# Kernel optimization log

Measured on AMD Instinct MI355X. Metric: run time of the kernel, lower is better.

The kernel has to match this reference:

```python
import jax, jax.numpy as jnp
import numpy as np
import math

D_MODEL = 1024
N_HEAD = 16
D_K = 64
D_V = 64
EPS = 1e-6


def setup_inputs() -> dict:
    key = jax.random.key(0)
    ks = jax.random.split(key, 10)
    B, S = 4, 2048
    inp = {
        'x_queries': jax.random.normal(ks[0], (B, S, D_MODEL), jnp.float32),
        'x_keys': jax.random.normal(ks[1], (B, S, D_MODEL), jnp.float32),
        'x_values': jax.random.normal(ks[2], (B, S, D_MODEL), jnp.float32),
        'mask': jax.random.randint(ks[3], (B, S, S), 0, 2, jnp.int32),
        # Linear(d_model, n_head*d_k, bias=False) weights stored as [in, out]
        'w_q': jax.random.normal(ks[4], (D_MODEL, N_HEAD * D_K), jnp.float32) * np.sqrt(2.0 / (D_MODEL + D_K)),
        'w_k': jax.random.normal(ks[5], (D_MODEL, N_HEAD * D_K), jnp.float32) * np.sqrt(2.0 / (D_MODEL + D_K)),
        'w_v': jax.random.normal(ks[6], (D_MODEL, N_HEAD * D_V), jnp.float32) * np.sqrt(2.0 / (D_MODEL + D_V)),
        'w_0': jax.random.normal(ks[7], (N_HEAD * D_V, D_MODEL), jnp.float32) * np.sqrt(2.0 / (N_HEAD * D_V + D_MODEL)),
        'gamma': jnp.ones((D_MODEL,), jnp.float32),
        'beta': jnp.zeros((D_MODEL,), jnp.float32),
    }
    return inp


def _layer_norm(x, gamma, beta, eps=EPS):
    # Matches the torch module: std with Bessel correction, eps added to std.
    mean = jnp.mean(x, axis=-1, keepdims=True)
    std = jnp.std(x, axis=-1, keepdims=True, ddof=1)
    return gamma * (x - mean) / (std + eps) + beta


def reference(x_queries, x_keys, x_values, mask, w_q, w_k, w_v, w_0, gamma, beta):
    B, Lq, _ = x_queries.shape
    residual = x_queries
    # Projections -> [B, L, H, D]
    Q = (x_queries @ w_q).reshape(B, Lq, N_HEAD, D_K)
    K = (x_keys @ w_k).reshape(B, x_keys.shape[1], N_HEAD, D_K)
    V = (x_values @ w_v).reshape(B, x_values.shape[1], N_HEAD, D_V)
    # Scaled dot-product attention (scores materialized as in the original bmm path)
    scores = jnp.einsum('bqhd,bkhd->bhqk', Q, K) / math.sqrt(D_K)
    # NOTE: original masked_fill uses eps (not -inf) where mask == 0
    scores = jnp.where(mask[:, None, :, :] == 0, EPS, scores)
    attn = jax.nn.softmax(scores, axis=-1)
    out = jnp.einsum('bhqk,bkhd->bqhd', attn, V).reshape(B, Lq, N_HEAD * D_V)
    out = out @ w_0
    return _layer_norm(out + residual, gamma, beta)
```

## Files before the change

### kernel.cpp

```cpp
#include <hip/hip_runtime.h>
#include <hip/hip_bf16.h>
#include <math.h>

#define DM 1024
#define NH 16
#define DK 64
#define BB 4
#define SS 2048
#define EPSV 1e-6f
#define NE ((size_t)BB * SS * DM)
#define MM ((size_t)DM * DM)
#define QSCALE 0.18033688011112042f

typedef __attribute__((ext_vector_type(8))) short short8;
typedef __attribute__((ext_vector_type(4))) float f32x4;

__device__ inline unsigned short f2bf(float x) {
  unsigned int u = __builtin_bit_cast(unsigned int, x);
  u += 0x7FFF + ((u >> 16) & 1);
  return (unsigned short)(u >> 16);
}
__device__ inline ushort4 f2bf4(float4 v) {
  ushort4 r;
  r.x = f2bf(v.x); r.y = f2bf(v.y); r.z = f2bf(v.z); r.w = f2bf(v.w);
  return r;
}

__device__ inline float fexp2(float x) {
#if __has_builtin(__builtin_amdgcn_exp2f)
  return __builtin_amdgcn_exp2f(x);
#else
  return exp2f(x);
#endif
}

__device__ inline unsigned cvtpk_bf16(float a, float b) {
  unsigned r;
  asm("v_cvt_pk_bf16_f32 %0, %1, %2" : "=v"(r) : "v"(a), "v"(b));
  return r;
}

__device__ inline void gl_lds16(const unsigned short* g, unsigned short* l) {
  __builtin_amdgcn_global_load_lds((const __attribute__((address_space(1))) void*)g,
                                   (__attribute__((address_space(3))) void*)l, 16, 0, 0);
}

__global__ __launch_bounds__(256) void cvt_x_k(const float* __restrict__ xq,
                                               const float* __restrict__ xk,
                                               const float* __restrict__ xv,
                                               unsigned short* __restrict__ oq,
                                               unsigned short* __restrict__ ok,
                                               unsigned short* __restrict__ ov) {
  const size_t NF4 = NE / 4;
  size_t g = (size_t)blockIdx.x * 256 + threadIdx.x;
  int t = (int)(g / NF4);
  size_t i = g - (size_t)t * NF4;
  const float* s = (t == 0) ? xq : (t == 1) ? xk : xv;
  unsigned short* d = (t == 0) ? oq : (t == 1) ? ok : ov;
  float4 v = ((const float4*)s)[i];
  ((ushort4*)d)[i] = f2bf4(v);
}

__global__ __launch_bounds__(256) void cvt_wT_k(const float* __restrict__ w0,
                                                const float* __restrict__ w1,
                                                const float* __restrict__ w2,
                                                const float* __restrict__ w3,
                                                unsigned short* __restrict__ o0,
                                                unsigned short* __restrict__ o1,
                                                unsigned short* __restrict__ o2,
                                                unsigned short* __restrict__ o3) {
  __shared__ float t[32][33];
  int z = blockIdx.z;
  const float* w = (z == 0) ? w0 : (z == 1) ? w1 : (z == 2) ? w2 : w3;
  unsigned short* o = (z == 0) ? o0 : (z == 1) ? o1 : (z == 2) ? o2 : o3;
  float sc = (z == 0) ? QSCALE : 1.0f;
  int n0 = blockIdx.x * 32, k0 = blockIdx.y * 32;
  int tx = threadIdx.x & 31, ty = threadIdx.x >> 5;
#pragma unroll
  for (int s = 0; s < 4; ++s) t[ty + s * 8][tx] = w[(size_t)(k0 + ty + s * 8) * DM + n0 + tx];
  __syncthreads();
#pragma unroll
  for (int s = 0; s < 4; ++s)
    o[(size_t)(n0 + ty + s * 8) * DM + k0 + tx] = f2bf(t[tx][ty + s * 8] * sc);
}

__global__ __launch_bounds__(256) void maskbits_k(const int* __restrict__ mask,
                                                  unsigned long long* __restrict__ bm) {
  const int total = BB * SS * (SS / 64);
  int lane = threadIdx.x & 63;
  int wid = (blockIdx.x * 256 + threadIdx.x) >> 6;
  int nw = (gridDim.x * 256) >> 6;
  for (int w = wid; w < total; w += nw) {
    int v = mask[(size_t)w * 64 + lane];
    unsigned long long bal = __ballot(v != 0);
    if (lane == 0) bm[w] = bal;
  }
}

__global__ __launch_bounds__(256) void vpack_k(const unsigned short* __restrict__ Vb,
                                               unsigned short* __restrict__ VP) {
  __shared__ unsigned short t[64][72];
  int b = blockIdx.z, h = blockIdx.y, kt = blockIdx.x;
  int tid = threadIdx.x;
#pragma unroll
  for (int p = 0; p < 2; ++p) {
    int idx = p * 256 + tid;
    int r = idx >> 3, cch = (idx & 7) * 8;
    short8 v = *(const short8*)&Vb[((size_t)b * SS + kt * 64 + r) * DM + h * DK + cch];
    *(short8*)&t[r][cch] = v;
  }
  __syncthreads();
  int o = tid >> 4, w0 = o & 3;
  int dcol = (o >> 2) * 16 + ((tid & 15) >> 1) * 2 + (tid & 1);
  unsigned short* dst =
      VP + (((size_t)b * NH + h) * (SS / 64) + kt) * 4096 + (size_t)tid * 8;
#pragma unroll
  for (int p = 0; p < 2; ++p) {
    union { short8 v; unsigned short u[8]; } pk;
#pragma unroll
    for (int j = 0; j < 8; ++j) {
      int srow = p * 32 + 16 * (j >> 2) + 4 * w0 + (j & 3);
      pk.u[j] = t[srow][dcol];
    }
    *(short8*)&dst[p * 2048] = pk.v;
  }
}

template <bool BF16OUT>
__global__ __launch_bounds__(256) void gemm_lds_k(const unsigned short* __restrict__ Abase,
                                                  const unsigned short* __restrict__ WTbase,
                                                  void* __restrict__ Cv, int M, int N, int K,
                                                  size_t zA, size_t zW, size_t zC) {
  __shared__ __align__(16) unsigned short As[128 * 32];
  __shared__ __align__(16) unsigned short Bs[128 * 32];
  const unsigned short* A = Abase + (size_t)blockIdx.z * zA;
  const unsigned short* WT = WTbase + (size_t)blockIdx.z * zW;
  int bm = blockIdx.y * 128, bn = blockIdx.x * 128;
  int tid = threadIdx.x, lane = tid & 63, w = tid >> 6;
  int quad = lane >> 4, c = lane & 15, wx = w & 1, wy = w >> 1;

  f32x4 acc[4][4];
#pragma unroll
  for (int mt = 0; mt < 4; ++mt)
#pragma unroll
    for (int nt = 0; nt < 4; ++nt)
#pragma unroll
      for (int r = 0; r < 4; ++r) acc[mt][nt][r] = 0.f;

  int srow = lane >> 2, scol = (lane & 3) * 8;
  const unsigned short* Ag = A + (size_t)(bm + w * 32 + srow) * K + scol;
  const unsigned short* Bg = WT + (size_t)(bn + w * 32 + srow) * K + scol;
  unsigned short* Al = &As[w * 32 * 32];
  unsigned short* Bl = &Bs[w * 32 * 32];

  for (int k0 = 0; k0 < K; k0 += 32) {
    gl_lds16(Ag + k0, Al);
    gl_lds16(Ag + (size_t)16 * K + k0, Al + 16 * 32);
    gl_lds16(Bg + k0, Bl);
    gl_lds16(Bg + (size_t)16 * K + k0, Bl + 16 * 32);
    __syncthreads();
    short8 af[4], bf[4];
#pragma unroll
    for (int mt = 0; mt < 4; ++mt) af[mt] = *(const short8*)&As[(wy * 64 + mt * 16 + c) * 32 + quad * 8];
#pragma unroll
    for (int nt = 0; nt < 4; ++nt) bf[nt] = *(const short8*)&Bs[(wx * 64 + nt * 16 + c) * 32 + quad * 8];
#pragma unroll
    for (int mt = 0; mt < 4; ++mt)
#pragma unroll
      for (int nt = 0; nt < 4; ++nt)
        acc[mt][nt] = __builtin_amdgcn_mfma_f32_16x16x32_bf16(af[mt], bf[nt], acc[mt][nt], 0, 0, 0);
    __syncthreads();
  }
#pragma unroll
  for (int mt = 0; mt < 4; ++mt)
#pragma unroll
    for (int nt = 0; nt < 4; ++nt)
#pragma unroll
      for (int r = 0; r < 4; ++r) {
        size_t idx = (size_t)blockIdx.z * zC +
                     (size_t)(bm + wy * 64 + mt * 16 + quad * 4 + r) * N + bn + wx * 64 + nt * 16 + c;
        if (BF16OUT)
          ((unsigned short*)Cv)[idx] = f2bf(acc[mt][nt][r]);
        else
          ((float*)Cv)[idx] = acc[mt][nt][r];
      }
}

__global__ __launch_bounds__(256) void attn_mfma_k(const unsigned short* __restrict__ Q,
                                                   const unsigned short* __restrict__ Kg,
                                                   const unsigned short* __restrict__ VP,
                                                   const unsigned long long* __restrict__ bm,
                                                   unsigned short* __restrict__ O) {
  __shared__ __align__(16) unsigned short Ks[2][64 * 64];
  __shared__ __align__(16) unsigned short Vs[2][64 * 64];
  int b = blockIdx.z, h = blockIdx.y, q0 = blockIdx.x * 64;
  int tid = threadIdx.x, lane = tid & 63, w = tid >> 6;
  int quad = lane >> 4, c = lane & 15;

  short8 qf[2];
  {
    const unsigned short* qp = Q + ((size_t)b * SS + q0 + w * 16 + c) * DM + h * DK + quad * 8;
    qf[0] = *(const short8*)qp;
    qf[1] = *(const short8*)(qp + 32);
  }
  const unsigned long long* bp = bm + ((size_t)b * SS + q0 + w * 16 + c) * (SS / 64);
  const int shq = quad * 4;

  short8 ones8;
#pragma unroll
  for (int j = 0; j < 8; ++j) ones8[j] = (short)0x3F80;

  f32x4 accO[4], lacc;
#pragma unroll
  for (int r = 0; r < 4; ++r) lacc[r] = 0.f;
#pragma unroll
  for (int dt = 0; dt < 4; ++dt)
#pragma unroll
    for (int r = 0; r < 4; ++r) accO[dt][r] = 0.f;

  int kr = tid >> 3;
  int scc = (tid & 7) ^ (kr & 7);
  const unsigned short* pK0 = Kg + ((size_t)b * SS + kr) * DM + h * DK + scc * 8;
  const unsigned short* pK1 = pK0 + (size_t)32 * DM;
  const unsigned short* pV0 =
      VP + ((size_t)b * NH + h) * (SS / 64) * 4096 + (size_t)tid * 8;
  const unsigned short* pV1 = pV0 + 2048;

  const int kfo0 = c * 64 + ((quad ^ (c & 7)) * 8);
  const int kfo1 = c * 64 + (((4 + quad) ^ (c & 7)) * 8);
  const int vfbase = quad * 128 + c * 8;

  const int NT = SS / 64;

  gl_lds16(pK0, &Ks[0][w * 512]);
  gl_lds16(pK1, &Ks[0][2048 + w * 512]);
  gl_lds16(pV0, &Vs[0][w * 512]);
  gl_lds16(pV1, &Vs[0][2048 + w * 512]);
  pK0 += (size_t)64 * DM; pK1 += (size_t)64 * DM;
  pV0 += 4096; pV1 += 4096;
  unsigned long long mw = bp[0];

  auto tile = [&](int buf, int kt) {
    __syncthreads();
    if (kt + 1 < NT) {
      gl_lds16(pK0, &Ks[buf ^ 1][w * 512]);
      gl_lds16(pK1, &Ks[buf ^ 1][2048 + w * 512]);
      gl_lds16(pV0, &Vs[buf ^ 1][w * 512]);
      gl_lds16(pV1, &Vs[buf ^ 1][2048 + w * 512]);
      pK0 += (size_t)64 * DM; pK1 += (size_t)64 * DM;
      pV0 += 4096; pV1 += 4096;
    }
    unsigned long long mw_next = (kt + 1 < NT) ? bp[kt + 1] : 0ull;

    f32x4 sacc[4];
#pragma unroll
    for (int nt = 0; nt < 4; ++nt) {
#pragma unroll
      for (int r = 0; r < 4; ++r) sacc[nt][r] = 0.f;
      short8 ka = *(const short8*)&Ks[buf][kfo0 + nt * 1024];
      short8 kb = *(const short8*)&Ks[buf][kfo1 + nt * 1024];
      sacc[nt] = __builtin_amdgcn_mfma_f32_16x16x32_bf16(ka, qf[0], sacc[nt], 0, 0, 0);
      sacc[nt] = __builtin_amdgcn_mfma_f32_16x16x32_bf16(kb, qf[1], sacc[nt], 0, 0, 0);
    }

    unsigned long long msh = mw >> shq;
    unsigned mlo = (unsigned)msh, mhi = (unsigned)(msh >> 32);
    unsigned padw[8];
#pragma unroll
    for (int nt = 0; nt < 4; ++nt) {
      unsigned msel = (nt & 2) ? mhi : mlo;
      const int bse = (nt & 1) * 16;
      float pv[4];
#pragma unroll
      for (int r = 0; r < 4; ++r) {
        float ex = fexp2(sacc[nt][r]);
        pv[r] = ((msel >> (bse + r)) & 1u) ? ex : 1.0f;
      }
      padw[nt * 2] = cvtpk_bf16(pv[0], pv[1]);
      padw[nt * 2 + 1] = cvtpk_bf16(pv[2], pv[3]);
    }
    mw = mw_next;

#pragma unroll
    for (int pkt = 0; pkt < 2; ++pkt) {
      union { unsigned u[4]; short8 s8; } pa;
#pragma unroll
      for (int i = 0; i < 4; ++i) pa.u[i] = padw[pkt * 4 + i];
      lacc = __builtin_amdgcn_mfma_f32_16x16x32_bf16(pa.s8, ones8, lacc, 0, 0, 0);
#pragma unroll
      for (int dt = 0; dt < 4; ++dt) {
        short8 vf = *(const short8*)&Vs[buf][(pkt * 4 + dt) * 512 + vfbase];
        accO[dt] = __builtin_amdgcn_mfma_f32_16x16x32_bf16(pa.s8, vf, accO[dt], 0, 0, 0);
      }
    }
  };

  for (int kt2 = 0; kt2 < NT; kt2 += 2) {
    tile(0, kt2);
    tile(1, kt2 + 1);
  }

  float inv[4];
#pragma unroll
  for (int r = 0; r < 4; ++r) inv[r] = 1.f / lacc[r];
#pragma unroll
  for (int dt = 0; dt < 4; ++dt)
#pragma unroll
    for (int r = 0; r < 4; ++r) {
      int q = q0 + w * 16 + quad * 4 + r;
      O[((size_t)b * SS + q) * DM + h * DK + dt * 16 + c] = f2bf(accO[dt][r] * inv[r]);
    }
}

__global__ __launch_bounds__(256) void ln_k(const float* __restrict__ P,
                                            const float* __restrict__ X,
                                            const float* __restrict__ gamma,
                                            const float* __restrict__ beta,
                                            float* __restrict__ out) {
  __shared__ float sm[4];
  int row = blockIdx.x, tid = threadIdx.x, w = tid >> 6;
  float4 p = ((const float4*)(P + (size_t)row * DM))[tid];
  float4 x = ((const float4*)(X + (size_t)row * DM))[tid];
  float4 v = make_float4(p.x + x.x, p.y + x.y, p.z + x.z, p.w + x.w);
  float s = (v.x + v.y) + (v.z + v.w);
#pragma unroll
  for (int off = 1; off < 64; off <<= 1) s += __shfl_xor(s, off);
  if ((tid & 63) == 0) sm[w] = s;
  __syncthreads();
  float mean = (sm[0] + sm[1] + sm[2] + sm[3]) * (1.f / DM);
  __syncthreads();
  float dx = v.x - mean, dy = v.y - mean, dz = v.z - mean, dw = v.w - mean;
  float s2 = (dx * dx + dy * dy) + (dz * dz + dw * dw);
#pragma unroll
  for (int off = 1; off < 64; off <<= 1) s2 += __shfl_xor(s2, off);
  if ((tid & 63) == 0) sm[w] = s2;
  __syncthreads();
  float var = (sm[0] + sm[1] + sm[2] + sm[3]) * (1.f / (DM - 1));
  float inv = 1.f / (sqrtf(var) + EPSV);
  float4 g = ((const float4*)gamma)[tid];
  float4 be = ((const float4*)beta)[tid];
  float4 y = make_float4(g.x * dx * inv + be.x, g.y * dy * inv + be.y,
                         g.z * dz * inv + be.z, g.w * dw * inv + be.w);
  ((float4*)(out + (size_t)row * DM))[tid] = y;
}

extern "C" void kernel_launch(void* const* d_in, const int* in_sizes, int n_in,
                              void* d_out, int out_size, void* d_ws, size_t ws_size,
                              hipStream_t stream) {
  const float* xq = (const float*)d_in[0];
  const float* xk = (const float*)d_in[1];
  const float* xv = (const float*)d_in[2];
  const int* mask = (const int*)d_in[3];
  const float* wq = (const float*)d_in[4];
  const float* wk = (const float*)d_in[5];
  const float* wv = (const float*)d_in[6];
  const float* w0 = (const float*)d_in[7];
  const float* gamma = (const float*)d_in[8];
  const float* beta = (const float*)d_in[9];
  float* out = (float*)d_out;

  unsigned short* xqb = (unsigned short*)d_ws;
  unsigned short* xkb = xqb + NE;
  unsigned short* xvb = xkb + NE;
  unsigned short* wTq = xvb + NE;
  unsigned short* wTk = wTq + MM;
  unsigned short* wTv = wTk + MM;
  unsigned short* wT0 = wTv + MM;
  unsigned short* Qb = wT0 + MM;
  unsigned short* Kb = Qb + NE;
  unsigned short* Vb = Kb + NE;
  unsigned short* AOb = Vb + NE;
  unsigned short* VPb = xvb;
  float* P = (float*)Qb;
  unsigned long long* bm = (unsigned long long*)d_out;

  const int M = BB * SS;
  cvt_x_k<<<(unsigned)(3 * (NE / 4) / 256), 256, 0, stream>>>(xq, xk, xv, xqb, xkb, xvb);
  cvt_wT_k<<<dim3(32, 32, 4), 256, 0, stream>>>(wq, wk, wv, w0, wTq, wTk, wTv, wT0);
  maskbits_k<<<256, 256, 0, stream>>>(mask, bm);
  gemm_lds_k<true><<<dim3(DM / 128, M / 128, 3), 256, 0, stream>>>(
      xqb, wTq, Qb, M, DM, DM, NE, MM, NE);
  vpack_k<<<dim3(SS / 64, NH, BB), 256, 0, stream>>>(Vb, VPb);
  attn_mfma_k<<<dim3(SS / 64, NH, BB), 256, 0, stream>>>(Qb, Kb, VPb, bm, AOb);
  gemm_lds_k<false><<<dim3(DM / 128, M / 128, 1), 256, 0, stream>>>(
      AOb, wT0, P, M, DM, DM, 0, 0, 0);
  ln_k<<<M, 256, 0, stream>>>(P, xq, gamma, beta, out);
}
```

Measured before the change: 551.2 us.

## Triple-buffer attention K/V loads and remap blocks for XCD-aware locality

The attention kernel moves from a double-buffered to a triple-buffered K/V LDS pipeline, using explicit vmcnt waits, raw barriers and sched_barriers so two tiles are in flight while one is computed. MFMA sections are raised with s_setprio. Both the GEMM and attention kernels remap linear block IDs so blocks landing on the same XCD (stride 8) handle neighbouring tiles, which is meant to improve L2 reuse. The changes add LDS use, which may lower occupancy, and rely on hardcoded grid shapes and vmcnt counts.

```diff
diff --git a/kernel.cpp b/kernel.cpp
--- a/kernel.cpp
+++ b/kernel.cpp
@@ -130,12 +130,15 @@
 __global__ __launch_bounds__(256) void gemm_lds_k(const unsigned short* __restrict__ Abase,
                                                   const unsigned short* __restrict__ WTbase,
                                                   void* __restrict__ Cv, int M, int N, int K,
-                                                  size_t zA, size_t zW, size_t zC) {
+                                                  size_t zA, size_t zW, size_t zC, int cpx) {
   __shared__ __align__(16) unsigned short As[128 * 32];
   __shared__ __align__(16) unsigned short Bs[128 * 32];
-  const unsigned short* A = Abase + (size_t)blockIdx.z * zA;
-  const unsigned short* WT = WTbase + (size_t)blockIdx.z * zW;
-  int bm = blockIdx.y * 128, bn = blockIdx.x * 128;
+  int dlin = (blockIdx.z * gridDim.y + blockIdx.y) * gridDim.x + blockIdx.x;
+  int l = (dlin & 7) * cpx + (dlin >> 3);
+  int bxs = l & 7, bys = (l >> 3) & 63, bzs = l >> 9;
+  const unsigned short* A = Abase + (size_t)bzs * zA;
+  const unsigned short* WT = WTbase + (size_t)bzs * zW;
+  int bm = bys * 128, bn = bxs * 128;
   int tid = threadIdx.x, lane = tid & 63, w = tid >> 6;
   int quad = lane >> 4, c = lane & 15, wx = w & 1, wy = w >> 1;
 
@@ -177,7 +180,7 @@
     for (int nt = 0; nt < 4; ++nt)
 #pragma unroll
       for (int r = 0; r < 4; ++r) {
-        size_t idx = (size_t)blockIdx.z * zC +
+        size_t idx = (size_t)bzs * zC +
                      (size_t)(bm + wy * 64 + mt * 16 + quad * 4 + r) * N + bn + wx * 64 + nt * 16 + c;
         if (BF16OUT)
           ((unsigned short*)Cv)[idx] = f2bf(acc[mt][nt][r]);
@@ -191,9 +194,13 @@
                                                    const unsigned short* __restrict__ VP,
                                                    const unsigned long long* __restrict__ bm,
                                                    unsigned short* __restrict__ O) {
-  __shared__ __align__(16) unsigned short Ks[2][64 * 64];
-  __shared__ __align__(16) unsigned short Vs[2][64 * 64];
-  int b = blockIdx.z, h = blockIdx.y, q0 = blockIdx.x * 64;
+  __shared__ __align__(16) unsigned short Ks[3][64 * 64];
+  __shared__ __align__(16) unsigned short Vs[3][64 * 64];
+  int dlin = (blockIdx.z * NH + blockIdx.y) * (SS / 64) + blockIdx.x;
+  int l = (dlin & 7) * 256 + (dlin >> 3);
+  int q0 = (l & 31) * 64;
+  int h = (l >> 5) & 15;
+  int b = l >> 9;
   int tid = threadIdx.x, lane = tid & 63, w = tid >> 6;
   int quad = lane >> 4, c = lane & 15;
 
@@ -209,6 +216,7 @@
   short8 ones8;
 #pragma unroll
   for (int j = 0; j < 8; ++j) ones8[j] = (short)0x3F80;
+  const f32x4 z4 = {0.f, 0.f, 0.f, 0.f};
 
   f32x4 accO[4], lacc;
 #pragma unroll
@@ -230,40 +238,39 @@
   const int kfo1 = c * 64 + (((4 + quad) ^ (c & 7)) * 8);
   const int vfbase = quad * 128 + c * 8;
 
-  const int NT = SS / 64;
-
-  gl_lds16(pK0, &Ks[0][w * 512]);
-  gl_lds16(pK1, &Ks[0][2048 + w * 512]);
-  gl_lds16(pV0, &Vs[0][w * 512]);
-  gl_lds16(pV1, &Vs[0][2048 + w * 512]);
-  pK0 += (size_t)64 * DM; pK1 += (size_t)64 * DM;
-  pV0 += 4096; pV1 += 4096;
-  unsigned long long mw = bp[0];
-
-  auto tile = [&](int buf, int kt) {
-    __syncthreads();
-    if (kt + 1 < NT) {
-      gl_lds16(pK0, &Ks[buf ^ 1][w * 512]);
-      gl_lds16(pK1, &Ks[buf ^ 1][2048 + w * 512]);
-      gl_lds16(pV0, &Vs[buf ^ 1][w * 512]);
-      gl_lds16(pV1, &Vs[buf ^ 1][2048 + w * 512]);
-      pK0 += (size_t)64 * DM; pK1 += (size_t)64 * DM;
-      pV0 += 4096; pV1 += 4096;
-    }
-    unsigned long long mw_next = (kt + 1 < NT) ? bp[kt + 1] : 0ull;
-
+#define MFENCE asm volatile("" ::: "memory")
+#define SYNCW(N)                                          \
+  do {                                                    \
+    asm volatile("s_waitcnt vmcnt(" #N ")" ::: "memory"); \
+    __builtin_amdgcn_s_barrier();                         \
+    __builtin_amdgcn_sched_barrier(0);                    \
+  } while (0)
+#define STAGE(i)                                   \
+  do {                                             \
+    gl_lds16(pK0, &Ks[i][w * 512]);                \
+    gl_lds16(pK1, &Ks[i][2048 + w * 512]);         \
+    gl_lds16(pV0, &Vs[i][w * 512]);                \
+    gl_lds16(pV1, &Vs[i][2048 + w * 512]);         \
+    pK0 += (size_t)64 * DM; pK1 += (size_t)64 * DM; \
+    pV0 += 4096; pV1 += 4096;                      \
+  } while (0)
+
+  unsigned long long mw, mwN;
+
+  auto compute = [&](const unsigned short* KsB, const unsigned short* VsB,
+                     unsigned long long mwv) {
     f32x4 sacc[4];
+    __builtin_amdgcn_s_setprio(1);
 #pragma unroll
     for (int nt = 0; nt < 4; ++nt) {
-#pragma unroll
-      for (int r = 0; r < 4; ++r) sacc[nt][r] = 0.f;
-      short8 ka = *(const short8*)&Ks[buf][kfo0 + nt * 1024];
-      short8 kb = *(const short8*)&Ks[buf][kfo1 + nt * 1024];
-      sacc[nt] = __builtin_amdgcn_mfma_f32_16x16x32_bf16(ka, qf[0], sacc[nt], 0, 0, 0);
+      short8 ka = *(const short8*)&KsB[kfo0 + nt * 1024];
+      short8 kb = *(const short8*)&KsB[kfo1 + nt * 1024];
+      sacc[nt] = __builtin_amdgcn_mfma_f32_16x16x32_bf16(ka, qf[0], z4, 0, 0, 0);
       sacc[nt] = __builtin_amdgcn_mfma_f32_16x16x32_bf16(kb, qf[1], sacc[nt], 0, 0, 0);
     }
-
-    unsigned long long msh = mw >> shq;
+    __builtin_amdgcn_s_setprio(0);
+
+    unsigned long long msh = mwv >> shq;
     unsigned mlo = (unsigned)msh, mhi = (unsigned)(msh >> 32);
     unsigned padw[8];
 #pragma unroll
@@ -279,8 +286,8 @@
       padw[nt * 2] = cvtpk_bf16(pv[0], pv[1]);
       padw[nt * 2 + 1] = cvtpk_bf16(pv[2], pv[3]);
     }
-    mw = mw_next;
-
+
+    __builtin_amdgcn_s_setprio(1);
 #pragma unroll
     for (int pkt = 0; pkt < 2; ++pkt) {
       union { unsigned u[4]; short8 s8; } pa;
@@ -289,16 +296,41 @@
       lacc = __builtin_amdgcn_mfma_f32_16x16x32_bf16(pa.s8, ones8, lacc, 0, 0, 0);
 #pragma unroll
       for (int dt = 0; dt < 4; ++dt) {
-        short8 vf = *(const short8*)&Vs[buf][(pkt * 4 + dt) * 512 + vfbase];
+        short8 vf = *(const short8*)&VsB[(pkt * 4 + dt) * 512 + vfbase];
         accO[dt] = __builtin_amdgcn_mfma_f32_16x16x32_bf16(pa.s8, vf, accO[dt], 0, 0, 0);
       }
     }
+    __builtin_amdgcn_s_setprio(0);
   };
 
-  for (int kt2 = 0; kt2 < NT; kt2 += 2) {
-    tile(0, kt2);
-    tile(1, kt2 + 1);
-  }
+  STAGE(0);
+  MFENCE;
+  mw = bp[0];
+  MFENCE;
+  STAGE(1);
+
+  for (int kt3 = 0; kt3 < 30; kt3 += 3) {
+    SYNCW(5); mwN = bp[kt3 + 1]; MFENCE; STAGE(2);
+    __builtin_amdgcn_sched_barrier(0);
+    compute(&Ks[0][0], &Vs[0][0], mw); mw = mwN;
+
+    SYNCW(5); mwN = bp[kt3 + 2]; MFENCE; STAGE(0);
+    __builtin_amdgcn_sched_barrier(0);
+    compute(&Ks[1][0], &Vs[1][0], mw); mw = mwN;
+
+    SYNCW(5); mwN = bp[kt3 + 3]; MFENCE; STAGE(1);
+    __builtin_amdgcn_sched_barrier(0);
+    compute(&Ks[2][0], &Vs[2][0], mw); mw = mwN;
+  }
+  SYNCW(5); mwN = bp[31]; MFENCE;
+  __builtin_amdgcn_sched_barrier(0);
+  compute(&Ks[0][0], &Vs[0][0], mw); mw = mwN;
+  SYNCW(1);
+  compute(&Ks[1][0], &Vs[1][0], mw);
+
+#undef MFENCE
+#undef SYNCW
+#undef STAGE
 
   float inv[4];
 #pragma unroll
@@ -379,10 +411,10 @@
   cvt_wT_k<<<dim3(32, 32, 4), 256, 0, stream>>>(wq, wk, wv, w0, wTq, wTk, wTv, wT0);
   maskbits_k<<<256, 256, 0, stream>>>(mask, bm);
   gemm_lds_k<true><<<dim3(DM / 128, M / 128, 3), 256, 0, stream>>>(
-      xqb, wTq, Qb, M, DM, DM, NE, MM, NE);
+      xqb, wTq, Qb, M, DM, DM, NE, MM, NE, 192);
   vpack_k<<<dim3(SS / 64, NH, BB), 256, 0, stream>>>(Vb, VPb);
   attn_mfma_k<<<dim3(SS / 64, NH, BB), 256, 0, stream>>>(Qb, Kb, VPb, bm, AOb);
   gemm_lds_k<false><<<dim3(DM / 128, M / 128, 1), 256, 0, stream>>>(
-      AOb, wT0, P, M, DM, DM, 0, 0, 0);
+      AOb, wT0, P, M, DM, DM, 0, 0, 0, 64);
   ln_k<<<M, 256, 0, stream>>>(P, xq, gamma, beta, out);
 }
```

Measured after the change: 542.8 us. About the same (-1.5%).
